# Performance work log

Measured on AMD Instinct MI355X. Metric: run time of the kernel, lower is better.

The kernel has to match this reference:

```python
import jax, jax.numpy as jnp
import numpy as np

E = 1024   # embedding_dim
H = 16     # heads
DK = 64    # key/query dim per head
DV = 64    # value dim per head
S = 2048   # seq len
B = 2      # batch


def setup_inputs() -> dict:
    key = jax.random.key(0)
    k0, k1, k2, k3, k4 = jax.random.split(key, 5)
    inputs = jax.random.normal(k0, (S, B, E), dtype=jnp.float32)
    # nn.Linear weight is [out, in]; we store transposed [in, out] for x @ W
    Wq = jax.random.normal(k1, (E, H * DK), dtype=jnp.float32) / np.sqrt(E)
    Wk = jax.random.normal(k2, (E, H * DK), dtype=jnp.float32) / np.sqrt(E)
    Wv = jax.random.normal(k3, (E, H * DV), dtype=jnp.float32) / np.sqrt(E)
    Wo = jax.random.normal(k4, (H * DV, E), dtype=jnp.float32) / np.sqrt(H * DV)
    return {"inputs": inputs, "Wq": Wq, "Wk": Wk, "Wv": Wv, "Wo": Wo}


def reference(inputs, Wq, Wk, Wv, Wo):
    # inputs: [S, B, E] (sequence-first, as implied by Permute(1,2,0,3))
    scale = jnp.sqrt(jnp.asarray(DK, dtype=inputs.dtype))
    q = (inputs @ Wq).reshape(S, B, H, DK).transpose(1, 2, 0, 3)  # [B,H,S,DK]
    k = (inputs @ Wk).reshape(S, B, H, DK).transpose(1, 2, 3, 0)  # [B,H,DK,S]
    v = (inputs @ Wv).reshape(S, B, H, DV).transpose(1, 2, 0, 3)  # [B,H,S,DV]
    attn = jax.nn.softmax((q @ k) / scale, axis=-1)               # [B,H,S,S]
    ctx = attn @ v                                                # [B,H,S,DV]
    # Transpose(1,2) -> [B,S,H,DV], Flatten -> [B,S,H*DV], Linear -> [B,S,E], Transpose(0,1) -> [S,B,E]
    out = ctx.transpose(0, 2, 1, 3).reshape(B, S, H * DV) @ Wo
    return out.transpose(1, 0, 2)  # [S, B, E]
```

## Files before the change

kernel.cpp:

```cpp
#include <hip/hip_runtime.h>
#include <hip/hip_bf16.h>

#define S_DIM 2048
#define B_DIM 2
#define E_DIM 1024
#define H_DIM 16
#define M_ROWS 4096

typedef __attribute__((ext_vector_type(8))) short bf16x8;
typedef __attribute__((ext_vector_type(4))) float f32x4;

__device__ inline unsigned short f2bf(float x) {
    unsigned int b = __float_as_uint(x);
    return (unsigned short)((b + 0x7fffu + ((b >> 16) & 1u)) >> 16);
}

#define GLD_LDS16(gsrc, ldst)                                                              \
    __builtin_amdgcn_global_load_lds((const __attribute__((address_space(1))) void*)(gsrc), \
                                     (__attribute__((address_space(3))) void*)(ldst), 16, 0, 0)

__global__ __launch_bounds__(256) void cast_x(const float* __restrict__ X,
                                              unsigned short* __restrict__ Xb) {
    int g = blockIdx.x * 256 + threadIdx.x;
    const float4* src = reinterpret_cast<const float4*>(X) + (size_t)g * 2;
    float4 v0 = src[0], v1 = src[1];
    union { unsigned short h[8]; int4 v; } u;
    u.h[0] = f2bf(v0.x); u.h[1] = f2bf(v0.y); u.h[2] = f2bf(v0.z); u.h[3] = f2bf(v0.w);
    u.h[4] = f2bf(v1.x); u.h[5] = f2bf(v1.y); u.h[6] = f2bf(v1.z); u.h[7] = f2bf(v1.w);
    *reinterpret_cast<int4*>(Xb + (size_t)g * 8) = u.v;
}

__global__ __launch_bounds__(256) void transpose_cast(
        const float* __restrict__ Wq, const float* __restrict__ Wk,
        const float* __restrict__ Wv, const float* __restrict__ Wo,
        unsigned short* __restrict__ Wqt, unsigned short* __restrict__ Wkt,
        unsigned short* __restrict__ Wvt, unsigned short* __restrict__ Wot) {
    const float* W = (blockIdx.z == 0) ? Wq : (blockIdx.z == 1) ? Wk
                   : (blockIdx.z == 2) ? Wv : Wo;
    unsigned short* Wt = (blockIdx.z == 0) ? Wqt : (blockIdx.z == 1) ? Wkt
                       : (blockIdx.z == 2) ? Wvt : Wot;
    const float scl = (blockIdx.z == 0) ? 0.125f : 1.0f;
    __shared__ float T[64][65];
    const int t = threadIdx.x;
    const int k0 = blockIdx.x * 64, n0 = blockIdx.y * 64;
#pragma unroll
    for (int p = 0; p < 4; ++p) {
        int r = p * 16 + (t >> 4), c4 = (t & 15) * 4;
        float4 v = *reinterpret_cast<const float4*>(&W[(size_t)(k0 + r) * E_DIM + n0 + c4]);
        T[r][c4] = v.x; T[r][c4 + 1] = v.y; T[r][c4 + 2] = v.z; T[r][c4 + 3] = v.w;
    }
    __syncthreads();
    const int nl = t >> 2, ks = (t & 3) * 16;
    union { unsigned short h[16]; int4 v[2]; } u;
#pragma unroll
    for (int i = 0; i < 16; ++i) u.h[i] = f2bf(T[ks + i][nl] * scl);
    int4* dst = reinterpret_cast<int4*>(&Wt[(size_t)(n0 + nl) * E_DIM + k0 + ks]);
    dst[0] = u.v[0]; dst[1] = u.v[1];
}

#define GEMM_BODY                                                                          \
    __shared__ int4 smem_i4[2048];                                                         \
    char* sm = reinterpret_cast<char*>(smem_i4);                                           \
    char* smA = sm; char* smB = sm + 16384;                                                \
    const int tid = threadIdx.x; const int lane = tid & 63; const int wid = tid >> 6;      \
    const int wr = (wid >> 1) * 64, wc = (wid & 1) * 64;                                   \
    const int r0 = blockIdx.x * 128, n0 = blockIdx.y * 128;                                \
    f32x4 acc[4][4] = {};                                                                  \
    const int srow = tid >> 3, sslot = tid & 7;                                            \
    for (int k0 = 0; k0 < E_DIM; k0 += 64) {                                               \
        __syncthreads();                                                                   \
        _Pragma("unroll") for (int p = 0; p < 4; ++p) {                                    \
            int row = p * 32 + srow;                                                       \
            int kc = k0 + ((sslot ^ (row & 7)) * 8);                                       \
            GLD_LDS16(&A[(size_t)(r0 + row) * E_DIM + kc], smA + p * 4096 + tid * 16);     \
            GLD_LDS16(&Bt[(size_t)(n0 + row) * E_DIM + kc], smB + p * 4096 + tid * 16);    \
        }                                                                                  \
        __syncthreads();                                                                   \
        _Pragma("unroll") for (int ks = 0; ks < 2; ++ks) {                                 \
            bf16x8 af[4], bfr[4];                                                          \
            _Pragma("unroll") for (int f = 0; f < 4; ++f) {                                \
                int ra = wr + f * 16 + (lane & 15);                                        \
                af[f] = *reinterpret_cast<bf16x8*>(smA + ra * 128 + (((ks * 4 + (lane >> 4)) ^ (ra & 7)) << 4)); \
                int rb = wc + f * 16 + (lane & 15);                                        \
                bfr[f] = *reinterpret_cast<bf16x8*>(smB + rb * 128 + (((ks * 4 + (lane >> 4)) ^ (rb & 7)) << 4)); \
            }                                                                              \
            _Pragma("unroll") for (int i = 0; i < 4; ++i)                                  \
                _Pragma("unroll") for (int j = 0; j < 4; ++j)                              \
                    acc[i][j] = __builtin_amdgcn_mfma_f32_16x16x32_bf16(af[i], bfr[j], acc[i][j], 0, 0, 0); \
        }                                                                                  \
    }

__global__ __launch_bounds__(256) void gemm_qkv(
        const unsigned short* __restrict__ A,
        const unsigned short* __restrict__ Wqt, const unsigned short* __restrict__ Wkt,
        const unsigned short* __restrict__ Wvt,
        unsigned short* __restrict__ Q, unsigned short* __restrict__ K,
        unsigned short* __restrict__ Vt) {
    const unsigned short* Bt = (blockIdx.z == 0) ? Wqt : (blockIdx.z == 1) ? Wkt : Wvt;
    GEMM_BODY
    unsigned short* O = (blockIdx.z == 0) ? Q : (blockIdx.z == 1) ? K : Vt;
    const int mode = blockIdx.z;
#pragma unroll
    for (int i = 0; i < 4; ++i)
#pragma unroll
    for (int j = 0; j < 4; ++j)
#pragma unroll
    for (int q = 0; q < 4; ++q) {
        int row = r0 + wr + i * 16 + (lane >> 4) * 4 + q;
        int col = n0 + wc + j * 16 + (lane & 15);
        int s = row >> 1, b = row & 1, h = col >> 6, d = col & 63;
        unsigned short v = f2bf(acc[i][j][q]);
        if (mode < 2) O[(((size_t)(b * H_DIM + h)) * S_DIM + s) * 64 + d] = v;
        else          O[(((size_t)(b * H_DIM + h)) * 64 + d) * S_DIM + s] = v;
    }
}

__global__ __launch_bounds__(256) void gemm_out(
        const unsigned short* __restrict__ A,
        const unsigned short* __restrict__ Bt, float* __restrict__ out) {
    GEMM_BODY
#pragma unroll
    for (int i = 0; i < 4; ++i)
#pragma unroll
    for (int j = 0; j < 4; ++j)
#pragma unroll
    for (int q = 0; q < 4; ++q) {
        int row = r0 + wr + i * 16 + (lane >> 4) * 4 + q;
        int b = row >> 11, s = row & 2047;
        int col = n0 + wc + j * 16 + (lane & 15);
        out[((size_t)(s * B_DIM + b)) * E_DIM + col] = acc[i][j][q];
    }
}

__global__ __launch_bounds__(512) void attn(
        const unsigned short* __restrict__ Q, const unsigned short* __restrict__ K,
        const unsigned short* __restrict__ Vt, unsigned short* __restrict__ ctx) {
    __shared__ int4 smem_i4[3072];
    char* sm = reinterpret_cast<char*>(smem_i4);
    char* smK = sm;
    char* smV = sm + 16384;
    char* smP = sm + 32768;
    const int tid = threadIdx.x, lane = tid & 63, wid = tid >> 6;
    const int bh = blockIdx.y;
    const int i0 = blockIdx.x * 128;
    const unsigned short* Qb = Q + (size_t)bh * S_DIM * 64;
    const unsigned short* Kb = K + (size_t)bh * S_DIM * 64;
    const unsigned short* Vb = Vt + (size_t)bh * 64 * S_DIM;
    char* smPw = smP + wid * 2048;

    bf16x8 qf[2];
#pragma unroll
    for (int ks = 0; ks < 2; ++ks) {
        int qrow = i0 + wid * 16 + (lane & 15);
        qf[ks] = *reinterpret_cast<const bf16x8*>(
            &Qb[(size_t)qrow * 64 + ks * 32 + (lane >> 4) * 8]);
    }

    f32x4 o[4] = {};
    float mrun = -INFINITY, lrun = 0.f;

    const int srow = tid >> 3, sslot = tid & 7;
    const int kc8 = (sslot ^ (srow & 7)) * 8;
    const int prow = lane & 15;
    const int xl = (lane & 48) | ((lane >> 4) * 4);

    GLD_LDS16(&Kb[(size_t)srow * 64 + kc8], smK + tid * 16);
    GLD_LDS16(&Vb[(size_t)srow * S_DIM + kc8], smV + tid * 16);

    int cur = 0;
    for (int t = 0; t < S_DIM / 64; ++t) {
        __syncthreads();
        if (t + 1 < S_DIM / 64) {
            int j1 = (t + 1) * 64;
            GLD_LDS16(&Kb[(size_t)(j1 + srow) * 64 + kc8], smK + (cur ^ 1) * 8192 + tid * 16);
            GLD_LDS16(&Vb[(size_t)srow * S_DIM + j1 + kc8], smV + (cur ^ 1) * 8192 + tid * 16);
        }
        char* K_ = smK + cur * 8192;
        char* V_ = smV + cur * 8192;

        f32x4 sv[4] = {};
        __builtin_amdgcn_s_setprio(1);
#pragma unroll
        for (int ks = 0; ks < 2; ++ks) {
            bf16x8 kf[4];
#pragma unroll
            for (int jf = 0; jf < 4; ++jf) {
                int r = jf * 16 + (lane & 15);
                kf[jf] = *reinterpret_cast<bf16x8*>(
                    K_ + r * 128 + (((ks * 4 + (lane >> 4)) ^ (r & 7)) << 4));
            }
#pragma unroll
            for (int jf = 0; jf < 4; ++jf)
                sv[jf] = __builtin_amdgcn_mfma_f32_16x16x32_bf16(kf[jf], qf[ks], sv[jf], 0, 0, 0);
        }
        __builtin_amdgcn_s_setprio(0);

        float ml = sv[0][0];
#pragma unroll
        for (int jf = 0; jf < 4; ++jf)
#pragma unroll
            for (int r = 0; r < 4; ++r) ml = fmaxf(ml, sv[jf][r]);
        ml = fmaxf(ml, __shfl_xor(ml, 16));
        ml = fmaxf(ml, __shfl_xor(ml, 32));
        if (__any(ml > mrun + 8.0f)) {
            float mn = fmaxf(mrun, ml);
            float al = __expf(mrun - mn);
            mrun = mn; lrun *= al;
            float al4[4];
#pragma unroll
            for (int q = 0; q < 4; ++q) al4[q] = __shfl(al, xl + q);
#pragma unroll
            for (int df = 0; df < 4; ++df)
#pragma unroll
                for (int q = 0; q < 4; ++q) o[df][q] *= al4[q];
        }
        float ls = 0.f;
        char* pbase = smPw + prow * 128;
#pragma unroll
        for (int jf = 0; jf < 4; ++jf) {
            float p0 = __expf(sv[jf][0] - mrun), p1 = __expf(sv[jf][1] - mrun);
            float p2 = __expf(sv[jf][2] - mrun), p3 = __expf(sv[jf][3] - mrun);
            ls += (p0 + p1) + (p2 + p3);
            unsigned int w0 = ((unsigned int)f2bf(p1) << 16) | f2bf(p0);
            unsigned int w1 = ((unsigned int)f2bf(p3) << 16) | f2bf(p2);
            int cb = jf * 32 + (lane >> 4) * 8;
            int byte = (((cb >> 4) ^ (prow & 7)) << 4) | (cb & 15);
            uint2 w; w.x = w0; w.y = w1;
            *reinterpret_cast<uint2*>(pbase + byte) = w;
        }
        ls += __shfl_xor(ls, 16);
        ls += __shfl_xor(ls, 32);
        lrun += ls;

        __builtin_amdgcn_s_setprio(1);
#pragma unroll
        for (int ks = 0; ks < 2; ++ks) {
            bf16x8 pf, vf[4];
            {
                int r = lane & 15;
                pf = *reinterpret_cast<bf16x8*>(
                    smPw + r * 128 + (((ks * 4 + (lane >> 4)) ^ (r & 7)) << 4));
            }
#pragma unroll
            for (int df = 0; df < 4; ++df) {
                int r = df * 16 + (lane & 15);
                vf[df] = *reinterpret_cast<bf16x8*>(
                    V_ + r * 128 + (((ks * 4 + (lane >> 4)) ^ (r & 7)) << 4));
            }
#pragma unroll
            for (int df = 0; df < 4; ++df)
                o[df] = __builtin_amdgcn_mfma_f32_16x16x32_bf16(pf, vf[df], o[df], 0, 0, 0);
        }
        __builtin_amdgcn_s_setprio(0);

        cur ^= 1;
    }

    float linv = 1.0f / lrun;
    float linv4[4];
#pragma unroll
    for (int q = 0; q < 4; ++q) linv4[q] = __shfl(linv, xl + q);
    const int b = bh >> 4, h = bh & 15;
#pragma unroll
    for (int q = 0; q < 4; ++q) {
        int row = i0 + wid * 16 + (lane >> 4) * 4 + q;
#pragma unroll
        for (int df = 0; df < 4; ++df) {
            int col = h * 64 + df * 16 + (lane & 15);
            ctx[((size_t)(b * S_DIM + row)) * E_DIM + col] = f2bf(o[df][q] * linv4[q]);
        }
    }
}

extern "C" void kernel_launch(void* const* d_in, const int* in_sizes, int n_in,
                              void* d_out, int out_size, void* d_ws, size_t ws_size,
                              hipStream_t stream) {
    const float* X  = (const float*)d_in[0];
    const float* Wq = (const float*)d_in[1];
    const float* Wk = (const float*)d_in[2];
    const float* Wv = (const float*)d_in[3];
    const float* Wo = (const float*)d_in[4];
    float* out = (float*)d_out;

    char* ws = (char*)d_ws;
    const size_t MB = (size_t)1 << 20;
    unsigned short* Xb  = (unsigned short*)(ws);
    unsigned short* Wqt = (unsigned short*)(ws +  8 * MB);
    unsigned short* Wkt = (unsigned short*)(ws + 10 * MB);
    unsigned short* Wvt = (unsigned short*)(ws + 12 * MB);
    unsigned short* Wot = (unsigned short*)(ws + 14 * MB);
    unsigned short* Qb  = (unsigned short*)(ws + 16 * MB);
    unsigned short* Kb  = (unsigned short*)(ws + 24 * MB);
    unsigned short* Vt  = (unsigned short*)(ws + 32 * MB);
    unsigned short* ctx = (unsigned short*)(ws + 40 * MB);

    cast_x<<<dim3(2048), 256, 0, stream>>>(X, Xb);
    transpose_cast<<<dim3(16, 16, 4), 256, 0, stream>>>(Wq, Wk, Wv, Wo, Wqt, Wkt, Wvt, Wot);
    gemm_qkv<<<dim3(32, 8, 3), 256, 0, stream>>>(Xb, Wqt, Wkt, Wvt, Qb, Kb, Vt);
    attn<<<dim3(16, 32), 512, 0, stream>>>(Qb, Kb, Vt, ctx);
    gemm_out<<<dim3(32, 8), 256, 0, stream>>>(ctx, Wot, out);
}
```

Measured before the change: 214.4 us.

## Merge prep kernels, stage QKV epilogue through LDS, tweak attention loop

Merges the input cast and the weight transpose-cast into a single prep launch. The QKV GEMM now reorders its A rows so each tile covers 64 sequence positions for both batches. Its epilogue stages bf16 results in swizzled LDS and writes coalesced 16-byte stores, replacing scattered 2-byte global stores, which matters most for the transposed V layout. The attention loop drops the buffer toggle variable and unrolls by 2, uses a shallower max-reduction tree, and switches to the hardware bf16 conversion intrinsic. These changes add LDS traffic and an extra sync in the epilogue, plus some register pressure from the unroll.

```diff
diff --git a/kernel.cpp b/kernel.cpp
--- a/kernel.cpp
+++ b/kernel.cpp
@@ -14,35 +14,40 @@
     unsigned int b = __float_as_uint(x);
     return (unsigned short)((b + 0x7fffu + ((b >> 16) & 1u)) >> 16);
 }
+__device__ inline unsigned short f2bfh(float x) {
+    __hip_bfloat16 h = __float2bfloat16(x);
+    return *reinterpret_cast<unsigned short*>(&h);
+}
 
 #define GLD_LDS16(gsrc, ldst)                                                              \
     __builtin_amdgcn_global_load_lds((const __attribute__((address_space(1))) void*)(gsrc), \
                                      (__attribute__((address_space(3))) void*)(ldst), 16, 0, 0)
 
-__global__ __launch_bounds__(256) void cast_x(const float* __restrict__ X,
-                                              unsigned short* __restrict__ Xb) {
-    int g = blockIdx.x * 256 + threadIdx.x;
-    const float4* src = reinterpret_cast<const float4*>(X) + (size_t)g * 2;
-    float4 v0 = src[0], v1 = src[1];
-    union { unsigned short h[8]; int4 v; } u;
-    u.h[0] = f2bf(v0.x); u.h[1] = f2bf(v0.y); u.h[2] = f2bf(v0.z); u.h[3] = f2bf(v0.w);
-    u.h[4] = f2bf(v1.x); u.h[5] = f2bf(v1.y); u.h[6] = f2bf(v1.z); u.h[7] = f2bf(v1.w);
-    *reinterpret_cast<int4*>(Xb + (size_t)g * 8) = u.v;
-}
-
-__global__ __launch_bounds__(256) void transpose_cast(
+__global__ __launch_bounds__(256) void prep(
+        const float* __restrict__ X,
         const float* __restrict__ Wq, const float* __restrict__ Wk,
         const float* __restrict__ Wv, const float* __restrict__ Wo,
+        unsigned short* __restrict__ Xb,
         unsigned short* __restrict__ Wqt, unsigned short* __restrict__ Wkt,
         unsigned short* __restrict__ Wvt, unsigned short* __restrict__ Wot) {
-    const float* W = (blockIdx.z == 0) ? Wq : (blockIdx.z == 1) ? Wk
-                   : (blockIdx.z == 2) ? Wv : Wo;
-    unsigned short* Wt = (blockIdx.z == 0) ? Wqt : (blockIdx.z == 1) ? Wkt
-                       : (blockIdx.z == 2) ? Wvt : Wot;
-    const float scl = (blockIdx.z == 0) ? 0.125f : 1.0f;
     __shared__ float T[64][65];
     const int t = threadIdx.x;
-    const int k0 = blockIdx.x * 64, n0 = blockIdx.y * 64;
+    if (blockIdx.x < 2048) {
+        int g = blockIdx.x * 256 + t;
+        const float4* src = reinterpret_cast<const float4*>(X) + (size_t)g * 2;
+        float4 v0 = src[0], v1 = src[1];
+        union { unsigned short h[8]; int4 v; } u;
+        u.h[0] = f2bf(v0.x); u.h[1] = f2bf(v0.y); u.h[2] = f2bf(v0.z); u.h[3] = f2bf(v0.w);
+        u.h[4] = f2bf(v1.x); u.h[5] = f2bf(v1.y); u.h[6] = f2bf(v1.z); u.h[7] = f2bf(v1.w);
+        *reinterpret_cast<int4*>(Xb + (size_t)g * 8) = u.v;
+        return;
+    }
+    int f = blockIdx.x - 2048;
+    int z = f >> 8, rem = f & 255;
+    const float* W = (z == 0) ? Wq : (z == 1) ? Wk : (z == 2) ? Wv : Wo;
+    unsigned short* Wt = (z == 0) ? Wqt : (z == 1) ? Wkt : (z == 2) ? Wvt : Wot;
+    const float scl = (z == 0) ? 0.125f : 1.0f;
+    const int k0 = (rem >> 4) * 64, n0 = (rem & 15) * 64;
 #pragma unroll
     for (int p = 0; p < 4; ++p) {
         int r = p * 16 + (t >> 4), c4 = (t & 15) * 4;
@@ -58,21 +63,22 @@
     dst[0] = u.v[0]; dst[1] = u.v[1];
 }
 
-#define GEMM_BODY                                                                          \
+#define GEMM_BODY(AROWE)                                                                   \
     __shared__ int4 smem_i4[2048];                                                         \
     char* sm = reinterpret_cast<char*>(smem_i4);                                           \
     char* smA = sm; char* smB = sm + 16384;                                                \
     const int tid = threadIdx.x; const int lane = tid & 63; const int wid = tid >> 6;      \
     const int wr = (wid >> 1) * 64, wc = (wid & 1) * 64;                                   \
-    const int r0 = blockIdx.x * 128, n0 = blockIdx.y * 128;                                \
+    const int n0 = blockIdx.y * 128;                                                       \
     f32x4 acc[4][4] = {};                                                                  \
     const int srow = tid >> 3, sslot = tid & 7;                                            \
     for (int k0 = 0; k0 < E_DIM; k0 += 64) {                                               \
         __syncthreads();                                                                   \
         _Pragma("unroll") for (int p = 0; p < 4; ++p) {                                    \
             int row = p * 32 + srow;                                                       \
+            int arow = (AROWE);                                                            \
             int kc = k0 + ((sslot ^ (row & 7)) * 8);                                       \
-            GLD_LDS16(&A[(size_t)(r0 + row) * E_DIM + kc], smA + p * 4096 + tid * 16);     \
+            GLD_LDS16(&A[(size_t)arow * E_DIM + kc], smA + p * 4096 + tid * 16);           \
             GLD_LDS16(&Bt[(size_t)(n0 + row) * E_DIM + kc], smB + p * 4096 + tid * 16);    \
         }                                                                                  \
         __syncthreads();                                                                   \
@@ -97,28 +103,66 @@
         unsigned short* __restrict__ Q, unsigned short* __restrict__ K,
         unsigned short* __restrict__ Vt) {
     const unsigned short* Bt = (blockIdx.z == 0) ? Wqt : (blockIdx.z == 1) ? Wkt : Wvt;
-    GEMM_BODY
-    unsigned short* O = (blockIdx.z == 0) ? Q : (blockIdx.z == 1) ? K : Vt;
+    GEMM_BODY(((int)blockIdx.x * 64 + (row & 63)) * 2 + (row >> 6))
+    const int sB = blockIdx.x * 64;
     const int mode = blockIdx.z;
-#pragma unroll
-    for (int i = 0; i < 4; ++i)
-#pragma unroll
-    for (int j = 0; j < 4; ++j)
-#pragma unroll
-    for (int q = 0; q < 4; ++q) {
-        int row = r0 + wr + i * 16 + (lane >> 4) * 4 + q;
-        int col = n0 + wc + j * 16 + (lane & 15);
-        int s = row >> 1, b = row & 1, h = col >> 6, d = col & 63;
-        unsigned short v = f2bf(acc[i][j][q]);
-        if (mode < 2) O[(((size_t)(b * H_DIM + h)) * S_DIM + s) * 64 + d] = v;
-        else          O[(((size_t)(b * H_DIM + h)) * 64 + d) * S_DIM + s] = v;
+    unsigned short* O = (mode == 0) ? Q : (mode == 1) ? K : Vt;
+    __syncthreads();
+    if (mode < 2) {
+#pragma unroll
+        for (int i = 0; i < 4; ++i)
+#pragma unroll
+        for (int q = 0; q < 4; ++q) {
+            int u = wr + i * 16 + (lane >> 4) * 4 + q;
+            int ub = u * 256, ux = (u & 15) << 4;
+#pragma unroll
+            for (int j = 0; j < 4; ++j) {
+                int n = wc + j * 16 + (lane & 15);
+                *reinterpret_cast<unsigned short*>(sm + ub + ((n * 2) ^ ux)) = f2bfh(acc[i][j][q]);
+            }
+        }
+    } else {
+#pragma unroll
+        for (int j = 0; j < 4; ++j) {
+            int n = wc + j * 16 + (lane & 15);
+            int nb = n * 256, nx = (n & 15) << 4;
+#pragma unroll
+            for (int i = 0; i < 4; ++i)
+#pragma unroll
+            for (int q = 0; q < 4; ++q) {
+                int u = wr + i * 16 + (lane >> 4) * 4 + q;
+                *reinterpret_cast<unsigned short*>(sm + nb + ((u * 2) ^ nx)) = f2bfh(acc[i][j][q]);
+            }
+        }
+    }
+    __syncthreads();
+    const int rr = tid >> 4, cb16 = (tid & 15) * 16;
+#pragma unroll
+    for (int pass = 0; pass < 8; ++pass) {
+        if (mode < 2) {
+            int u = pass * 16 + rr;
+            int4 v = *reinterpret_cast<int4*>(sm + u * 256 + (cb16 ^ ((u & 15) << 4)));
+            int cg = n0 + (cb16 >> 1);
+            int h = cg >> 6, d = cg & 63;
+            int s = sB + (u & 63), b = u >> 6;
+            *reinterpret_cast<int4*>(&O[(((size_t)(b * 16 + h)) * 2048 + s) * 64 + d]) = v;
+        } else {
+            int n = pass * 16 + rr;
+            int4 v = *reinterpret_cast<int4*>(sm + n * 256 + (cb16 ^ ((n & 15) << 4)));
+            int cg = n0 + n;
+            int h = cg >> 6, d = cg & 63;
+            int u0 = cb16 >> 1;
+            int b = u0 >> 6, s = sB + (u0 & 63);
+            *reinterpret_cast<int4*>(&O[(((size_t)(b * 16 + h)) * 64 + d) * 2048 + s]) = v;
+        }
     }
 }
 
 __global__ __launch_bounds__(256) void gemm_out(
         const unsigned short* __restrict__ A,
         const unsigned short* __restrict__ Bt, float* __restrict__ out) {
-    GEMM_BODY
+    GEMM_BODY((int)blockIdx.x * 128 + row)
+    const int r0 = blockIdx.x * 128;
 #pragma unroll
     for (int i = 0; i < 4; ++i)
 #pragma unroll
@@ -167,16 +211,16 @@
     GLD_LDS16(&Kb[(size_t)srow * 64 + kc8], smK + tid * 16);
     GLD_LDS16(&Vb[(size_t)srow * S_DIM + kc8], smV + tid * 16);
 
-    int cur = 0;
+#pragma unroll 2
     for (int t = 0; t < S_DIM / 64; ++t) {
         __syncthreads();
         if (t + 1 < S_DIM / 64) {
             int j1 = (t + 1) * 64;
-            GLD_LDS16(&Kb[(size_t)(j1 + srow) * 64 + kc8], smK + (cur ^ 1) * 8192 + tid * 16);
-            GLD_LDS16(&Vb[(size_t)srow * S_DIM + j1 + kc8], smV + (cur ^ 1) * 8192 + tid * 16);
-        }
-        char* K_ = smK + cur * 8192;
-        char* V_ = smV + cur * 8192;
+            GLD_LDS16(&Kb[(size_t)(j1 + srow) * 64 + kc8], smK + ((t & 1) ^ 1) * 8192 + tid * 16);
+            GLD_LDS16(&Vb[(size_t)srow * S_DIM + j1 + kc8], smV + ((t & 1) ^ 1) * 8192 + tid * 16);
+        }
+        char* K_ = smK + (t & 1) * 8192;
+        char* V_ = smV + (t & 1) * 8192;
 
         f32x4 sv[4] = {};
         __builtin_amdgcn_s_setprio(1);
@@ -195,11 +239,14 @@
         }
         __builtin_amdgcn_s_setprio(0);
 
-        float ml = sv[0][0];
-#pragma unroll
-        for (int jf = 0; jf < 4; ++jf)
-#pragma unroll
-            for (int r = 0; r < 4; ++r) ml = fmaxf(ml, sv[jf][r]);
+        float m0 = fmaxf(fmaxf(sv[0][0], sv[0][1]), sv[0][2]);
+        float m1 = fmaxf(fmaxf(sv[0][3], sv[1][0]), sv[1][1]);
+        float m2 = fmaxf(fmaxf(sv[1][2], sv[1][3]), sv[2][0]);
+        float m3 = fmaxf(fmaxf(sv[2][1], sv[2][2]), sv[2][3]);
+        float m4 = fmaxf(fmaxf(sv[3][0], sv[3][1]), sv[3][2]);
+        float ml = fmaxf(fmaxf(m0, m1), m2);
+        ml = fmaxf(fmaxf(ml, m3), m4);
+        ml = fmaxf(ml, sv[3][3]);
         ml = fmaxf(ml, __shfl_xor(ml, 16));
         ml = fmaxf(ml, __shfl_xor(ml, 32));
         if (__any(ml > mrun + 8.0f)) {
@@ -221,8 +268,8 @@
             float p0 = __expf(sv[jf][0] - mrun), p1 = __expf(sv[jf][1] - mrun);
             float p2 = __expf(sv[jf][2] - mrun), p3 = __expf(sv[jf][3] - mrun);
             ls += (p0 + p1) + (p2 + p3);
-            unsigned int w0 = ((unsigned int)f2bf(p1) << 16) | f2bf(p0);
-            unsigned int w1 = ((unsigned int)f2bf(p3) << 16) | f2bf(p2);
+            unsigned int w0 = ((unsigned int)f2bfh(p1) << 16) | f2bfh(p0);
+            unsigned int w1 = ((unsigned int)f2bfh(p3) << 16) | f2bfh(p2);
             int cb = jf * 32 + (lane >> 4) * 8;
             int byte = (((cb >> 4) ^ (prow & 7)) << 4) | (cb & 15);
             uint2 w; w.x = w0; w.y = w1;
@@ -252,8 +299,6 @@
                 o[df] = __builtin_amdgcn_mfma_f32_16x16x32_bf16(pf, vf[df], o[df], 0, 0, 0);
         }
         __builtin_amdgcn_s_setprio(0);
-
-        cur ^= 1;
     }
 
     float linv = 1.0f / lrun;
@@ -267,7 +312,7 @@
 #pragma unroll
         for (int df = 0; df < 4; ++df) {
             int col = h * 64 + df * 16 + (lane & 15);
-            ctx[((size_t)(b * S_DIM + row)) * E_DIM + col] = f2bf(o[df][q] * linv4[q]);
+            ctx[((size_t)(b * S_DIM + row)) * E_DIM + col] = f2bfh(o[df][q] * linv4[q]);
         }
     }
 }
@@ -294,8 +339,7 @@
     unsigned short* Vt  = (unsigned short*)(ws + 32 * MB);
     unsigned short* ctx = (unsigned short*)(ws + 40 * MB);
 
-    cast_x<<<dim3(2048), 256, 0, stream>>>(X, Xb);
-    transpose_cast<<<dim3(16, 16, 4), 256, 0, stream>>>(Wq, Wk, Wv, Wo, Wqt, Wkt, Wvt, Wot);
+    prep<<<dim3(3072), 256, 0, stream>>>(X, Wq, Wk, Wv, Wo, Xb, Wqt, Wkt, Wvt, Wot);
     gemm_qkv<<<dim3(32, 8, 3), 256, 0, stream>>>(Xb, Wqt, Wkt, Wvt, Qb, Kb, Vt);
     attn<<<dim3(16, 32), 512, 0, stream>>>(Qb, Kb, Vt, ctx);
     gemm_out<<<dim3(32, 8), 256, 0, stream>>>(ctx, Wot, out);
```

Measured after the change: 197.2 us. -8.0%, faster.
